# Performance work log

Hardware: AMD Instinct MI355X
Metric: run time of the kernel (lower is better)

The kernel has to match this reference:

```python
import jax, jax.numpy as jnp
import numpy as np

INPUT, HIDDEN, OUTPUT = 128, 256, 128
BATCH, SEQ = 64, 2048


def setup_inputs() -> dict:
    key = jax.random.key(0)
    ks = jax.random.split(key, 7)
    s_ih = 1.0 / np.sqrt(HIDDEN)
    x = jax.random.normal(ks[0], (BATCH, SEQ, INPUT), dtype=jnp.float32)
    W_ih = jax.random.uniform(ks[1], (HIDDEN, INPUT), jnp.float32, -s_ih, s_ih)
    W_hh = jax.random.uniform(ks[2], (HIDDEN, HIDDEN), jnp.float32, -s_ih, s_ih)
    b_ih = jax.random.uniform(ks[3], (HIDDEN,), jnp.float32, -s_ih, s_ih)
    b_hh = jax.random.uniform(ks[4], (HIDDEN,), jnp.float32, -s_ih, s_ih)
    s_fc = 1.0 / np.sqrt(HIDDEN)
    W_fc = jax.random.uniform(ks[5], (OUTPUT, HIDDEN), jnp.float32, -s_fc, s_fc)
    b_fc = jax.random.uniform(ks[6], (OUTPUT,), jnp.float32, -s_fc, s_fc)
    return {"x": x, "W_ih": W_ih, "W_hh": W_hh, "b_ih": b_ih,
            "b_hh": b_hh, "W_fc": W_fc, "b_fc": b_fc}


def reference(x, W_ih, W_hh, b_ih, b_hh, W_fc, b_fc):
    B = x.shape[0]
    # Precompute input projections for all timesteps: [S, B, H]
    xp = jnp.einsum('bsi,hi->sbh', x, W_ih) + b_ih + b_hh
    h0 = jnp.zeros((B, W_hh.shape[0]), dtype=x.dtype)

    def step(h, xp_t):
        h = jnp.tanh(xp_t + h @ W_hh.T)
        return h, None

    hT, _ = jax.lax.scan(step, h0, xp)
    return hT @ W_fc.T + b_fc
```

## Files before the change

### kernel.cpp

```cpp
#include <hip/hip_runtime.h>
#include <hip/hip_bf16.h>
#include <hip/hip_fp16.h>


#define S_LEN 2048
#define B_SZ  64
#define IN_D  128
#define HID   256
#define OUT_D 128

typedef _Float16 half2_t __attribute__((ext_vector_type(2)));
typedef _Float16 half8_t __attribute__((ext_vector_type(8)));
typedef float    f32x4   __attribute__((ext_vector_type(4)));

#if __has_builtin(__builtin_amdgcn_fdot2)
#define FDOT2(a, b, c) __builtin_amdgcn_fdot2((a), (b), (c), false)
#else
#define FDOT2(a, b, c) ((c) + (float)(a).x * (float)(b).x + (float)(a).y * (float)(b).y)
#endif

#if __has_builtin(__builtin_amdgcn_exp2f)
#define EXP2F(x) __builtin_amdgcn_exp2f(x)
#else
#define EXP2F(x) exp2f(x)
#endif

__global__ __launch_bounds__(256) void xproj_kernel(
    const float* __restrict__ x, const float* __restrict__ W_ih,
    const float* __restrict__ b_ih, const float* __restrict__ b_hh,
    _Float16* __restrict__ xp)
{
    const int lane = threadIdx.x & 63;
    const int wave = threadIdx.x >> 6;
    const int m0 = (blockIdx.x * 4 + wave) * 16;
    const int n0 = blockIdx.y * 16;
    const int idx16 = lane & 15;
    const int kq = lane >> 4;

    f32x4 acc = {0.f, 0.f, 0.f, 0.f};

    #pragma unroll
    for (int sl = 0; sl < 4; ++sl) {
        const int koff = sl * 32 + kq * 8;
        const float4* ap = (const float4*)(x + (size_t)(m0 + idx16) * IN_D + koff);
        float4 a0 = ap[0], a1 = ap[1];
        const float4* bp = (const float4*)(W_ih + (size_t)(n0 + idx16) * IN_D + koff);
        float4 b0 = bp[0], b1 = bp[1];
        half8_t af = {(_Float16)a0.x, (_Float16)a0.y, (_Float16)a0.z, (_Float16)a0.w,
                      (_Float16)a1.x, (_Float16)a1.y, (_Float16)a1.z, (_Float16)a1.w};
        half8_t bf = {(_Float16)b0.x, (_Float16)b0.y, (_Float16)b0.z, (_Float16)b0.w,
                      (_Float16)b1.x, (_Float16)b1.y, (_Float16)b1.z, (_Float16)b1.w};
        acc = __builtin_amdgcn_mfma_f32_16x16x32_f16(af, bf, acc, 0, 0, 0);
    }

    const float bias = b_ih[n0 + idx16] + b_hh[n0 + idx16];
    #pragma unroll
    for (int r = 0; r < 4; ++r) {
        const int m = m0 + kq * 4 + r;
        const int bb = m >> 11;
        const int ss = m & 2047;
        xp[((size_t)ss * B_SZ + bb) * HID + n0 + idx16] = (_Float16)(acc[r] + bias);
    }
}

__global__ __launch_bounds__(256) void rnn_kernel(
    const _Float16* __restrict__ xp, const float* __restrict__ W_hh,
    const float* __restrict__ W_fc, const float* __restrict__ b_fc,
    float* __restrict__ out)
{
    const int b = blockIdx.x;
    const int j = threadIdx.x;

    __shared__ __align__(16) _Float16 hbuf[2][HID];

    half2_t w[128];
    {
        const float4* wr = (const float4*)(W_hh + (size_t)j * HID);
        #pragma unroll
        for (int c = 0; c < 64; ++c) {
            float4 v = wr[c];
            w[2 * c]     = half2_t{(_Float16)v.x, (_Float16)v.y};
            w[2 * c + 1] = half2_t{(_Float16)v.z, (_Float16)v.w};
        }
    }

    hbuf[0][j] = (_Float16)0.f;

    const _Float16* xpb = xp + (size_t)b * HID + j;
    _Float16 p0 = xpb[0];
    _Float16 p1 = xpb[(size_t)B_SZ * HID];

    __syncthreads();

    for (int t = 0; t < S_LEN; ++t) {
        const int rb = t & 1;
        float acc = 0.f;
        const float4* hp = (const float4*)hbuf[rb];
        #pragma unroll
        for (int c = 0; c < 32; ++c) {
            float4 hv = hp[c];
            union { float f; half2_t h; } u0, u1, u2, u3;
            u0.f = hv.x; u1.f = hv.y; u2.f = hv.z; u3.f = hv.w;
            acc = FDOT2(w[4 * c + 0], u0.h, acc);
            acc = FDOT2(w[4 * c + 1], u1.h, acc);
            acc = FDOT2(w[4 * c + 2], u2.h, acc);
            acc = FDOT2(w[4 * c + 3], u3.h, acc);
        }

        const float xv = (float)p0;
        p0 = p1;
        if (t + 2 < S_LEN) p1 = xpb[(size_t)(t + 2) * B_SZ * HID];

        const float z = acc + xv;
        const float e = EXP2F(z * 2.8853900817779268f);
        const float th = 1.f - 2.f / (e + 1.f);

        hbuf[rb ^ 1][j] = (_Float16)th;
        __syncthreads();
    }

    if (j < OUT_D) {
        float acc2 = b_fc[j];
        const float4* wp = (const float4*)(W_fc + (size_t)j * HID);
        const _Float16* hf = hbuf[0];
        #pragma unroll 8
        for (int c = 0; c < 64; ++c) {
            float4 wv = wp[c];
            acc2 += wv.x * (float)hf[4 * c + 0] + wv.y * (float)hf[4 * c + 1] +
                    wv.z * (float)hf[4 * c + 2] + wv.w * (float)hf[4 * c + 3];
        }
        out[(size_t)b * OUT_D + j] = acc2;
    }
}

extern "C" void kernel_launch(void* const* d_in, const int* in_sizes, int n_in,
                              void* d_out, int out_size, void* d_ws, size_t ws_size,
                              hipStream_t stream) {
    const float* x    = (const float*)d_in[0];
    const float* W_ih = (const float*)d_in[1];
    const float* W_hh = (const float*)d_in[2];
    const float* b_ih = (const float*)d_in[3];
    const float* b_hh = (const float*)d_in[4];
    const float* W_fc = (const float*)d_in[5];
    const float* b_fc = (const float*)d_in[6];
    float* outp = (float*)d_out;

    _Float16* xp_ws = (_Float16*)d_ws;

    dim3 gA(S_LEN * B_SZ / 64, HID / 16, 1);
    xproj_kernel<<<gA, 256, 0, stream>>>(x, W_ih, b_ih, b_hh, xp_ws);

    rnn_kernel<<<B_SZ, HID, 0, stream>>>(xp_ws, W_hh, W_fc, b_fc, outp);
}
```

Baseline: 1.575 ms.

## Restructure input projection for A-fragment reuse, batch-major xp, split dot chains

The projection kernel now loads and converts each x row tile once into registers and loops over all 16 output column tiles, instead of launching a separate block per column tile that reloads x. The xp workspace layout changes from seq-major to batch-major, so each recurrent block reads contiguous memory for its batch. The recurrent dot product is split into four independent accumulators to shorten the dependent FDOT2 chain on the serial critical path. The prefetch branch is replaced by a clamped index. The projection grid has fewer blocks and each block does more sequential work, and the altered summation order changes rounding slightly.

```diff
diff --git a/kernel.cpp b/kernel.cpp
--- a/kernel.cpp
+++ b/kernel.cpp
@@ -30,36 +30,39 @@
     const float* __restrict__ b_ih, const float* __restrict__ b_hh,
     _Float16* __restrict__ xp)
 {
-    const int lane = threadIdx.x & 63;
-    const int wave = threadIdx.x >> 6;
-    const int m0 = (blockIdx.x * 4 + wave) * 16;
-    const int n0 = blockIdx.y * 16;
+    const int lane  = threadIdx.x & 63;
+    const int wave  = threadIdx.x >> 6;
+    const int r0    = blockIdx.x * 64 + wave * 16;
     const int idx16 = lane & 15;
-    const int kq = lane >> 4;
+    const int kq    = lane >> 4;
 
-    f32x4 acc = {0.f, 0.f, 0.f, 0.f};
-
+    half8_t afr[4];
     #pragma unroll
     for (int sl = 0; sl < 4; ++sl) {
-        const int koff = sl * 32 + kq * 8;
-        const float4* ap = (const float4*)(x + (size_t)(m0 + idx16) * IN_D + koff);
+        const float4* ap = (const float4*)(x + (size_t)(r0 + idx16) * IN_D + sl * 32 + kq * 8);
         float4 a0 = ap[0], a1 = ap[1];
-        const float4* bp = (const float4*)(W_ih + (size_t)(n0 + idx16) * IN_D + koff);
-        float4 b0 = bp[0], b1 = bp[1];
-        half8_t af = {(_Float16)a0.x, (_Float16)a0.y, (_Float16)a0.z, (_Float16)a0.w,
-                      (_Float16)a1.x, (_Float16)a1.y, (_Float16)a1.z, (_Float16)a1.w};
-        half8_t bf = {(_Float16)b0.x, (_Float16)b0.y, (_Float16)b0.z, (_Float16)b0.w,
-                      (_Float16)b1.x, (_Float16)b1.y, (_Float16)b1.z, (_Float16)b1.w};
-        acc = __builtin_amdgcn_mfma_f32_16x16x32_f16(af, bf, acc, 0, 0, 0);
+        afr[sl] = half8_t{(_Float16)a0.x, (_Float16)a0.y, (_Float16)a0.z, (_Float16)a0.w,
+                          (_Float16)a1.x, (_Float16)a1.y, (_Float16)a1.z, (_Float16)a1.w};
     }
 
-    const float bias = b_ih[n0 + idx16] + b_hh[n0 + idx16];
-    #pragma unroll
-    for (int r = 0; r < 4; ++r) {
-        const int m = m0 + kq * 4 + r;
-        const int bb = m >> 11;
-        const int ss = m & 2047;
-        xp[((size_t)ss * B_SZ + bb) * HID + n0 + idx16] = (_Float16)(acc[r] + bias);
+    #pragma unroll 2
+    for (int nc = 0; nc < 16; ++nc) {
+        const int n0 = nc * 16;
+        f32x4 acc = {0.f, 0.f, 0.f, 0.f};
+        #pragma unroll
+        for (int sl = 0; sl < 4; ++sl) {
+            const float4* bp = (const float4*)(W_ih + (size_t)(n0 + idx16) * IN_D + sl * 32 + kq * 8);
+            float4 b0 = bp[0], b1 = bp[1];
+            half8_t bf = {(_Float16)b0.x, (_Float16)b0.y, (_Float16)b0.z, (_Float16)b0.w,
+                          (_Float16)b1.x, (_Float16)b1.y, (_Float16)b1.z, (_Float16)b1.w};
+            acc = __builtin_amdgcn_mfma_f32_16x16x32_f16(afr[sl], bf, acc, 0, 0, 0);
+        }
+        const float bias = b_ih[n0 + idx16] + b_hh[n0 + idx16];
+        #pragma unroll
+        for (int r = 0; r < 4; ++r) {
+            const int m = r0 + kq * 4 + r;
+            xp[(size_t)m * HID + n0 + idx16] = (_Float16)(acc[r] + bias);
+        }
     }
 }
 
@@ -86,30 +89,32 @@
 
     hbuf[0][j] = (_Float16)0.f;
 
-    const _Float16* xpb = xp + (size_t)b * HID + j;
+    const _Float16* xpb = xp + (size_t)b * S_LEN * HID + j;
     _Float16 p0 = xpb[0];
-    _Float16 p1 = xpb[(size_t)B_SZ * HID];
+    _Float16 p1 = xpb[HID];
 
     __syncthreads();
 
     for (int t = 0; t < S_LEN; ++t) {
         const int rb = t & 1;
-        float acc = 0.f;
+        float a0 = 0.f, a1 = 0.f, a2 = 0.f, a3 = 0.f;
         const float4* hp = (const float4*)hbuf[rb];
         #pragma unroll
         for (int c = 0; c < 32; ++c) {
             float4 hv = hp[c];
             union { float f; half2_t h; } u0, u1, u2, u3;
             u0.f = hv.x; u1.f = hv.y; u2.f = hv.z; u3.f = hv.w;
-            acc = FDOT2(w[4 * c + 0], u0.h, acc);
-            acc = FDOT2(w[4 * c + 1], u1.h, acc);
-            acc = FDOT2(w[4 * c + 2], u2.h, acc);
-            acc = FDOT2(w[4 * c + 3], u3.h, acc);
+            a0 = FDOT2(w[4 * c + 0], u0.h, a0);
+            a1 = FDOT2(w[4 * c + 1], u1.h, a1);
+            a2 = FDOT2(w[4 * c + 2], u2.h, a2);
+            a3 = FDOT2(w[4 * c + 3], u3.h, a3);
         }
+        const float acc = (a0 + a1) + (a2 + a3);
 
         const float xv = (float)p0;
         p0 = p1;
-        if (t + 2 < S_LEN) p1 = xpb[(size_t)(t + 2) * B_SZ * HID];
+        const int tn = (t + 2 < S_LEN) ? (t + 2) : (S_LEN - 1);
+        p1 = xpb[(size_t)tn * HID];
 
         const float z = acc + xv;
         const float e = EXP2F(z * 2.8853900817779268f);
@@ -147,7 +152,7 @@
 
     _Float16* xp_ws = (_Float16*)d_ws;
 
-    dim3 gA(S_LEN * B_SZ / 64, HID / 16, 1);
+    dim3 gA(S_LEN * B_SZ / 64, 1, 1);
     xproj_kernel<<<gA, 256, 0, stream>>>(x, W_ih, b_ih, b_hh, xp_ws);
 
     rnn_kernel<<<B_SZ, HID, 0, stream>>>(xp_ws, W_hh, W_fc, b_fc, outp);
```

New measurement: 1.387 ms. -11.9%, faster.
